# Kernel optimization log

Hardware: AMD Instinct MI355X
Metric: run time of the kernel (lower is better)

Reference implementation:

```python
import jax, jax.numpy as jnp
import numpy as np

BETA = 0.25
B, D, H, W = 32, 256, 32, 32
K = 1024


def setup_inputs() -> dict:
    key = jax.random.key(0)
    k1, k2 = jax.random.split(key)
    inputs = jax.random.normal(k1, (B, D, H, W), dtype=jnp.float32)
    # torch init: uniform(-1/K, 1/K)
    codebook = jax.random.uniform(k2, (K, D), dtype=jnp.float32,
                                  minval=-1.0 / K, maxval=1.0 / K)
    return {"inputs": inputs, "codebook": codebook}


def reference(inputs, codebook):
    b, d, h, w = inputs.shape
    # (B, C, H, W) -> (B*H*W, D)
    x = inputs.transpose(0, 2, 3, 1).reshape(b * h * w, d)
    # Squared Euclidean distances; argmin is identical to cdist argmin.
    x2 = jnp.sum(x * x, axis=1, keepdims=True)            # (N, 1)
    c2 = jnp.sum(codebook * codebook, axis=1)             # (K,)
    d2 = x2 - 2.0 * (x @ codebook.T) + c2[None, :]        # (N, K)
    idx = jnp.argmin(d2, axis=1)                          # (N,)
    q = codebook[idx].reshape(b, h, w, d).transpose(0, 3, 1, 2)  # (B, D, H, W)

    q_loss = jnp.mean((q - jax.lax.stop_gradient(inputs)) ** 2)
    e_loss = jnp.mean((jax.lax.stop_gradient(q) - inputs) ** 2)
    vq_loss = q_loss + BETA * e_loss

    # straight-through estimator
    quantized = inputs + jax.lax.stop_gradient(q - inputs)
    return quantized, q_loss, e_loss, vq_loss, idx.reshape(b, h, w)
```

## Files before the change

kernel.cpp:

```cpp
#include <hip/hip_runtime.h>
#include <cstdint>

typedef float floatx4 __attribute__((ext_vector_type(4)));
typedef _Float16 half8 __attribute__((ext_vector_type(8)));
typedef _Float16 half4v __attribute__((ext_vector_type(4)));

#define D_DIM 256
#define HW 1024
#define K_CODES 1024
#define NPIX 32768
#define NELEM 8388608

#define OFF_QLOSS 8388608
#define OFF_ELOSS 8388609
#define OFF_VQ    8388610
#define OFF_IDX   8388611

#define WS_C2      0
#define WS_CNT     4096
#define WS_LFIX    4160
#define WS_PART    4224
#define WS_FLAGPX  8320
#define WS_FLAGTOP 41088
#define WS_CBS     303232
#define FLAG_CAP   8192

#define MARGIN 2.5e-4f

__device__ __forceinline__ float np_pairwise_sq_256(const float* __restrict__ a, int stride) {
    float half[2];
#pragma unroll
    for (int h = 0; h < 2; ++h) {
        const float* p = a + (size_t)(h * 128) * stride;
        float r[8];
#pragma unroll
        for (int j = 0; j < 8; ++j) { float t = p[(size_t)j * stride]; r[j] = __fmul_rn(t, t); }
        for (int i = 8; i < 128; i += 8)
#pragma unroll
            for (int j = 0; j < 8; ++j) {
                float t = p[(size_t)(i + j) * stride];
                r[j] = __fadd_rn(r[j], __fmul_rn(t, t));
            }
        half[h] = __fadd_rn(__fadd_rn(__fadd_rn(r[0], r[1]), __fadd_rn(r[2], r[3])),
                            __fadd_rn(__fadd_rn(r[4], r[5]), __fadd_rn(r[6], r[7])));
    }
    return __fadd_rn(half[0], half[1]);
}

__global__ __launch_bounds__(256) void prep_kernel(const float* __restrict__ cb,
                                                   _Float16* __restrict__ cbs,
                                                   float* __restrict__ c2,
                                                   int* __restrict__ cnt,
                                                   double* __restrict__ lossFix) {
    int b = blockIdx.x;
    if (b < 256) {
        int idx = b * 256 + threadIdx.x;
        int c = idx >> 6;
        int d = (idx & 63) * 4;
        int s = d >> 5, q = (d >> 3) & 3, j0 = d & 7;
        int half = c >> 9, ch = (c >> 4) & 31, l15 = c & 15;
        int lane = q * 16 + l15;
        size_t o = ((((size_t)(half * 32 + ch) * 8 + s) * 64 + lane) * 8 + j0);
        floatx4 v = *(const floatx4*)(cb + (size_t)c * D_DIM + d);
        half4v h;
#pragma unroll
        for (int j = 0; j < 4; ++j) h[j] = (_Float16)(v[j] * 1024.0f);
        *(half4v*)(cbs + o) = h;
    } else {
        if (b == 256 && threadIdx.x == 0) *cnt = 0;
        if (b == 257 && threadIdx.x == 0) *lossFix = 0.0;
        int k = (b - 256) * 256 + threadIdx.x;
        c2[k] = np_pairwise_sq_256(cb + (size_t)k * D_DIM, 1);
    }
}

__device__ __forceinline__ void ins4v(float v, int k, float* S, int* I) {
    if (v < S[3]) {
        S[3] = v; I[3] = k;
#pragma unroll
        for (int j = 3; j > 0; --j) {
            if (S[j] < S[j - 1]) {
                float ts = S[j]; S[j] = S[j - 1]; S[j - 1] = ts;
                int   ti = I[j]; I[j] = I[j - 1]; I[j - 1] = ti;
            }
        }
    }
}

__global__ __launch_bounds__(256, 2) void gemm_swz(
        const float* __restrict__ x, const float* __restrict__ cb,
        const _Float16* __restrict__ cbs, const float* __restrict__ c2,
        float* __restrict__ out_idx, float* __restrict__ out_q,
        double* __restrict__ partials, int* __restrict__ cnt,
        int* __restrict__ flagPx, floatx4* __restrict__ flagTop) {
    __shared__ float scr[4][32 * 65];
    __shared__ int sidx[64];
    __shared__ double sredd[4];

    const int t = threadIdx.x;
    const int w = t >> 6;
    const int l = t & 63;
    const int l15 = l & 15;
    const int q = l >> 4;
    const int pxg = w >> 1;
    const int half = w & 1;
    const int px0 = blockIdx.x * 64;
    const int bimg = px0 >> 10;
    const int hwb = (px0 & 1023) + pxg * 32;
    const float* xb = x + (size_t)bimg * (D_DIM * HW);

    half8 A[2][8];
#pragma unroll
    for (int r = 0; r < 2; ++r) {
        float tmp[64];
#pragma unroll
        for (int s = 0; s < 8; ++s)
#pragma unroll
            for (int j = 0; j < 8; ++j)
                tmp[s * 8 + j] = xb[(size_t)(s * 32 + q * 8 + j) * HW + hwb + r * 16 + l15];
#pragma unroll
        for (int s = 0; s < 8; ++s) {
            half8 h;
#pragma unroll
            for (int j = 0; j < 8; ++j) h[j] = (_Float16)tmp[s * 8 + j];
            A[r][s] = h;
        }
    }

    const _Float16* base = cbs + (size_t)half * 131072;
    half8 B[4][8];
#pragma unroll
    for (int s = 0; s < 8; ++s) {
        B[0][s] = *(const half8*)(base + (size_t)s * 512 + l * 8);
        B[1][s] = *(const half8*)(base + 4096 + (size_t)s * 512 + l * 8);
    }
    float c2b[4];
    c2b[0] = c2[half * 512 + l15];
    c2b[1] = c2[half * 512 + 16 + l15];

    float m1[2][4], m2[2][4]; int i1[2][4], i2[2][4];
#pragma unroll
    for (int r = 0; r < 2; ++r)
#pragma unroll
        for (int a = 0; a < 4; ++a) {
            m1[r][a] = INFINITY; m2[r][a] = INFINITY; i1[r][a] = 0; i2[r][a] = 0;
        }

#pragma unroll 4
    for (int ch = 0; ch < 32; ++ch) {
        const int cur = ch & 3;
        if (ch < 30) {
            const int pf = (ch + 2) & 3;
            const _Float16* nb = base + (size_t)(ch + 2) * 4096;
#pragma unroll
            for (int s = 0; s < 8; ++s)
                B[pf][s] = *(const half8*)(nb + (size_t)s * 512 + l * 8);
            c2b[pf] = c2[half * 512 + (ch + 2) * 16 + l15];
        }
        floatx4 ac[2][2];
#pragma unroll
        for (int r = 0; r < 2; ++r)
#pragma unroll
            for (int h = 0; h < 2; ++h) ac[r][h] = floatx4{0.f, 0.f, 0.f, 0.f};
#pragma unroll
        for (int s = 0; s < 4; ++s) {
            ac[0][0] = __builtin_amdgcn_mfma_f32_16x16x32_f16(A[0][s],     B[cur][s],     ac[0][0], 0, 0, 0);
            ac[1][0] = __builtin_amdgcn_mfma_f32_16x16x32_f16(A[1][s],     B[cur][s],     ac[1][0], 0, 0, 0);
            ac[0][1] = __builtin_amdgcn_mfma_f32_16x16x32_f16(A[0][s + 4], B[cur][s + 4], ac[0][1], 0, 0, 0);
            ac[1][1] = __builtin_amdgcn_mfma_f32_16x16x32_f16(A[1][s + 4], B[cur][s + 4], ac[1][1], 0, 0, 0);
        }
        const int code = half * 512 + ch * 16 + l15;
        const float c2cur = c2b[cur];
#pragma unroll
        for (int r = 0; r < 2; ++r)
#pragma unroll
            for (int a = 0; a < 4; ++a) {
                float dot = ac[r][0][a] + ac[r][1][a];
                float s = fmaf(-0.001953125f, dot, c2cur);
                if (s < m1[r][a]) { m2[r][a] = m1[r][a]; i2[r][a] = i1[r][a]; m1[r][a] = s; i1[r][a] = code; }
                else if (s < m2[r][a]) { m2[r][a] = s; i2[r][a] = code; }
            }
    }

    const int part = half * 16 + l15;
#pragma unroll
    for (int r = 0; r < 2; ++r)
#pragma unroll
        for (int a = 0; a < 4; ++a) {
            int px = pxg * 32 + r * 16 + q * 4 + a;
            int o = part * 65 + px;
            scr[0][o] = m1[r][a];
            scr[1][o] = __int_as_float(i1[r][a]);
            scr[2][o] = m2[r][a];
            scr[3][o] = __int_as_float(i2[r][a]);
        }
    __syncthreads();
    if (t < 64) {
        float S[4] = {INFINITY, INFINITY, INFINITY, INFINITY};
        int   I[4] = {0x7fffffff, 0x7fffffff, 0x7fffffff, 0x7fffffff};
        for (int p = 0; p < 32; ++p) {
            int o = p * 65 + t;
            ins4v(scr[0][o], __float_as_int(scr[1][o]), S, I);
            ins4v(scr[2][o], __float_as_int(scr[3][o]), S, I);
        }
        int P = px0 + t;
        sidx[t] = I[0];
        out_idx[P] = (float)I[0];
        if (S[1] - S[0] <= MARGIN) {
            int pos = atomicAdd(cnt, 1);
            if (pos < FLAG_CAP) {
                flagPx[pos] = P;
                flagTop[2 * pos]     = floatx4{S[0], (float)I[0], S[1], (float)I[1]};
                flagTop[2 * pos + 1] = floatx4{S[2], (float)I[2], S[3], (float)I[3]};
            }
        }
    }
    __syncthreads();

    {
        const int dq = t >> 6;
        const int pxl = t & 63;
        const int myidx = sidx[pxl];
        const int hwofs = (px0 & 1023) + pxl;
        const float* xcol = x + (size_t)bimg * (D_DIM * HW) + hwofs;
        float* qcol = out_q + (size_t)bimg * (D_DIM * HW) + hwofs;
        const floatx4* crow = (const floatx4*)(cb + (size_t)myidx * D_DIM) + dq * 16;
        float lsum = 0.f;
#pragma unroll
        for (int i = 0; i < 16; ++i) {
            floatx4 cv = crow[i];
            int dbase = dq * 64 + i * 4;
#pragma unroll
            for (int j = 0; j < 4; ++j) {
                size_t off = (size_t)(dbase + j) * HW;
                float xv = xcol[off];
                qcol[off] = cv[j];
                float df = cv[j] - xv;
                lsum = fmaf(df, df, lsum);
            }
        }
        double ds = (double)lsum;
#pragma unroll
        for (int off = 32; off > 0; off >>= 1) ds += __shfl_down(ds, off);
        if (l == 0) sredd[w] = ds;
    }
    __syncthreads();
    if (t == 0) partials[blockIdx.x] = sredd[0] + sredd[1] + sredd[2] + sredd[3];
}

__global__ __launch_bounds__(256) void rescore_fix(
        const float* __restrict__ x, const float* __restrict__ cb,
        const float* __restrict__ c2, const int* __restrict__ cnt,
        const int* __restrict__ flagPx, const floatx4* __restrict__ flagTop,
        float* __restrict__ out_idx, float* __restrict__ out_q,
        double* __restrict__ lossFix) {
    const int wglobal = blockIdx.x * 4 + (threadIdx.x >> 6);
    const int l = threadIdx.x & 63;
    int n = *cnt; if (n > FLAG_CAP) n = FLAG_CAP;
    for (int i = wglobal; i < n; i += 1024) {
        int P = flagPx[i];
        floatx4 ta = flagTop[2 * i], tb = flagTop[2 * i + 1];
        float s1 = ta[0];
        float cs[4] = {ta[0], ta[2], tb[0], tb[2]};
        int   ck[4] = {(int)ta[1], (int)ta[3], (int)tb[1], (int)tb[3]};
        int nc = 1;
        while (nc < 4 && cs[nc] - s1 <= MARGIN) ++nc;

        const size_t colbase = (size_t)(P >> 10) * (D_DIM * HW) + (P & 1023);
        const float* xcol = x + colbase;

        float rj = 0.f;
        if (l < 16) {
            int h = l >> 3, j = l & 7;
            const float* p = xcol + (size_t)(h * 128) * HW;
            float v0 = p[(size_t)j * HW];
            rj = __fmul_rn(v0, v0);
            for (int ii = 1; ii < 16; ++ii) {
                float v = p[(size_t)(ii * 8 + j) * HW];
                rj = __fadd_rn(rj, __fmul_rn(v, v));
            }
        }
        float r0 = __shfl(rj, 0), r1 = __shfl(rj, 1), r2 = __shfl(rj, 2), r3 = __shfl(rj, 3);
        float r4 = __shfl(rj, 4), r5 = __shfl(rj, 5), r6 = __shfl(rj, 6), r7 = __shfl(rj, 7);
        float h0 = __fadd_rn(__fadd_rn(__fadd_rn(r0, r1), __fadd_rn(r2, r3)),
                             __fadd_rn(__fadd_rn(r4, r5), __fadd_rn(r6, r7)));
        r0 = __shfl(rj, 8); r1 = __shfl(rj, 9); r2 = __shfl(rj, 10); r3 = __shfl(rj, 11);
        r4 = __shfl(rj, 12); r5 = __shfl(rj, 13); r6 = __shfl(rj, 14); r7 = __shfl(rj, 15);
        float h1 = __fadd_rn(__fadd_rn(__fadd_rn(r0, r1), __fadd_rn(r2, r3)),
                             __fadd_rn(__fadd_rn(r4, r5), __fadd_rn(r6, r7)));
        float x2 = __fadd_rn(h0, h1);

        float xv[4];
#pragma unroll
        for (int u = 0; u < 4; ++u) xv[u] = xcol[(size_t)(l + u * 64) * HW];
        double accd[4] = {0.0, 0.0, 0.0, 0.0};
        for (int jc = 0; jc < nc; ++jc) {
            const float* cr = cb + (size_t)ck[jc] * D_DIM;
            double a = 0.0;
#pragma unroll
            for (int u = 0; u < 4; ++u) a += (double)xv[u] * (double)cr[l + u * 64];
#pragma unroll
            for (int off = 32; off > 0; off >>= 1) a += __shfl_xor(a, off);
            accd[jc] = a;
        }
        float bd = INFINITY; int bi = 0x7fffffff;
        for (int jc = 0; jc < nc; ++jc) {
            float mm = (float)accd[jc];
            float t1 = __fsub_rn(x2, __fmul_rn(2.0f, mm));
            float Dq = __fadd_rn(t1, c2[ck[jc]]);
            if (Dq < bd || (Dq == bd && ck[jc] < bi)) { bd = Dq; bi = ck[jc]; }
        }
        int oldI = (int)ta[1];
        if (l == 0) out_idx[P] = (float)bi;
        if (bi != oldI) {
            const float* cn = cb + (size_t)bi * D_DIM;
            const float* co = cb + (size_t)oldI * D_DIM;
            float* qcol = out_q + colbase;
            double dd = 0.0;
#pragma unroll
            for (int u = 0; u < 4; ++u) {
                int d = l + u * 64;
                float cnd = cn[d], cod = co[d];
                double dn = (double)cnd - (double)xv[u];
                double do_ = (double)cod - (double)xv[u];
                dd += dn * dn - do_ * do_;
                qcol[(size_t)d * HW] = cnd;
            }
#pragma unroll
            for (int off = 32; off > 0; off >>= 1) dd += __shfl_xor(dd, off);
            if (l == 0) atomicAdd(lossFix, dd);
        }
    }
}

__global__ __launch_bounds__(64) void finalize_loss(const double* __restrict__ partials,
                                                    const double* __restrict__ lossFix,
                                                    float* __restrict__ out) {
    double s = 0.0;
    for (int i = threadIdx.x; i < 512; i += 64) s += partials[i];
#pragma unroll
    for (int off = 32; off > 0; off >>= 1) s += __shfl_down(s, off);
    if (threadIdx.x == 0) {
        double m = (s + *lossFix) / (double)NELEM;
        out[OFF_QLOSS] = (float)m;
        out[OFF_ELOSS] = (float)m;
        out[OFF_VQ]    = (float)(1.25 * m);
    }
}

extern "C" void kernel_launch(void* const* d_in, const int* in_sizes, int n_in,
                              void* d_out, int out_size, void* d_ws, size_t ws_size,
                              hipStream_t stream) {
    const float* x  = (const float*)d_in[0];
    const float* cb = (const float*)d_in[1];
    float* out = (float*)d_out;
    char* ws = (char*)d_ws;

    float*    c2      = (float*)(ws + WS_C2);
    int*      cnt     = (int*)(ws + WS_CNT);
    double*   lossFix = (double*)(ws + WS_LFIX);
    double*   partials= (double*)(ws + WS_PART);
    int*      flagPx  = (int*)(ws + WS_FLAGPX);
    floatx4*  flagTop = (floatx4*)(ws + WS_FLAGTOP);
    _Float16* cbs     = (_Float16*)(ws + WS_CBS);

    prep_kernel<<<260, 256, 0, stream>>>(cb, cbs, c2, cnt, lossFix);
    gemm_swz<<<NPIX / 64, 256, 0, stream>>>(x, cb, cbs, c2, out + OFF_IDX, out,
                                            partials, cnt, flagPx, flagTop);
    rescore_fix<<<256, 256, 0, stream>>>(x, cb, c2, cnt, flagPx, flagTop,
                                         out + OFF_IDX, out, lossFix);
    finalize_loss<<<1, 64, 0, stream>>>(partials, lossFix, out);
}
```

Before: 170.3 us.

## Split quantize/loss epilogue into own kernel and fold finalize into rescore

Moves the codebook gather, quantized-output write and loss partial sum out of the GEMM kernel into a separate quantize_loss_kernel with 1024 smaller blocks. The finalize_loss launch is removed; the last rescore_fix block, found through an atomic done counter, reduces the partials. The aim is to shorten the register- and LDS-heavy GEMM kernel's tail and drop one launch. In exchange, the indices are re-read from global memory and one extra kernel is added.

New measurement: 193.9 us. 1.14x slower.

```diff
diff --git a/kernel.cpp b/kernel.cpp
--- a/kernel.cpp
+++ b/kernel.cpp
@@ -18,11 +18,12 @@
 
 #define WS_C2      0
 #define WS_CNT     4096
-#define WS_LFIX    4160
-#define WS_PART    4224
-#define WS_FLAGPX  8320
-#define WS_FLAGTOP 41088
-#define WS_CBS     303232
+#define WS_DONE    4160
+#define WS_LFIX    4224
+#define WS_PART    4288
+#define WS_FLAGPX  12480
+#define WS_FLAGTOP 45248
+#define WS_CBS     307392
 #define FLAG_CAP   8192
 
 #define MARGIN 2.5e-4f
@@ -51,7 +52,8 @@
                                                    _Float16* __restrict__ cbs,
                                                    float* __restrict__ c2,
                                                    int* __restrict__ cnt,
-                                                   double* __restrict__ lossFix) {
+                                                   double* __restrict__ lossFix,
+                                                   int* __restrict__ done) {
     int b = blockIdx.x;
     if (b < 256) {
         int idx = b * 256 + threadIdx.x;
@@ -69,6 +71,7 @@
     } else {
         if (b == 256 && threadIdx.x == 0) *cnt = 0;
         if (b == 257 && threadIdx.x == 0) *lossFix = 0.0;
+        if (b == 258 && threadIdx.x == 0) *done = 0;
         int k = (b - 256) * 256 + threadIdx.x;
         c2[k] = np_pairwise_sq_256(cb + (size_t)k * D_DIM, 1);
     }
@@ -88,14 +91,11 @@
 }
 
 __global__ __launch_bounds__(256, 2) void gemm_swz(
-        const float* __restrict__ x, const float* __restrict__ cb,
-        const _Float16* __restrict__ cbs, const float* __restrict__ c2,
-        float* __restrict__ out_idx, float* __restrict__ out_q,
-        double* __restrict__ partials, int* __restrict__ cnt,
-        int* __restrict__ flagPx, floatx4* __restrict__ flagTop) {
+        const float* __restrict__ x, const _Float16* __restrict__ cbs,
+        const float* __restrict__ c2, float* __restrict__ out_idx,
+        int* __restrict__ cnt, int* __restrict__ flagPx,
+        floatx4* __restrict__ flagTop) {
     __shared__ float scr[4][32 * 65];
-    __shared__ int sidx[64];
-    __shared__ double sredd[4];
 
     const int t = threadIdx.x;
     const int w = t >> 6;
@@ -204,7 +204,6 @@
             ins4v(scr[2][o], __float_as_int(scr[3][o]), S, I);
         }
         int P = px0 + t;
-        sidx[t] = I[0];
         out_idx[P] = (float)I[0];
         if (S[1] - S[0] <= MARGIN) {
             int pos = atomicAdd(cnt, 1);
@@ -215,37 +214,42 @@
             }
         }
     }
+}
+
+__global__ __launch_bounds__(256) void quantize_loss_kernel(
+        const float* __restrict__ x, const float* __restrict__ cb,
+        const float* __restrict__ out_idx, float* __restrict__ out_q,
+        double* __restrict__ partials) {
+    const int t = threadIdx.x;
+    const int pxl = t & 31;
+    const int dg = t >> 5;
+    const int P = blockIdx.x * 32 + pxl;
+    const int bimg = P >> 10, hw = P & 1023;
+    const float* xb = x + (size_t)bimg * D_DIM * HW + hw;
+    float* qb = out_q + (size_t)bimg * D_DIM * HW + hw;
+    const int myidx = (int)out_idx[P];
+    const floatx4* crow = (const floatx4*)(cb + (size_t)myidx * D_DIM) + dg * 8;
+    float lsum = 0.f;
+#pragma unroll
+    for (int i = 0; i < 8; ++i) {
+        floatx4 cv = crow[i];
+        int dbase = dg * 32 + i * 4;
+#pragma unroll
+        for (int j = 0; j < 4; ++j) {
+            size_t off = (size_t)(dbase + j) * HW;
+            float xv = xb[off];
+            qb[off] = cv[j];
+            float df = cv[j] - xv;
+            lsum = fmaf(df, df, lsum);
+        }
+    }
+    double ds = (double)lsum;
+#pragma unroll
+    for (int off = 32; off > 0; off >>= 1) ds += __shfl_down(ds, off);
+    __shared__ double sred[4];
+    if ((t & 63) == 0) sred[t >> 6] = ds;
     __syncthreads();
-
-    {
-        const int dq = t >> 6;
-        const int pxl = t & 63;
-        const int myidx = sidx[pxl];
-        const int hwofs = (px0 & 1023) + pxl;
-        const float* xcol = x + (size_t)bimg * (D_DIM * HW) + hwofs;
-        float* qcol = out_q + (size_t)bimg * (D_DIM * HW) + hwofs;
-        const floatx4* crow = (const floatx4*)(cb + (size_t)myidx * D_DIM) + dq * 16;
-        float lsum = 0.f;
-#pragma unroll
-        for (int i = 0; i < 16; ++i) {
-            floatx4 cv = crow[i];
-            int dbase = dq * 64 + i * 4;
-#pragma unroll
-            for (int j = 0; j < 4; ++j) {
-                size_t off = (size_t)(dbase + j) * HW;
-                float xv = xcol[off];
-                qcol[off] = cv[j];
-                float df = cv[j] - xv;
-                lsum = fmaf(df, df, lsum);
-            }
-        }
-        double ds = (double)lsum;
-#pragma unroll
-        for (int off = 32; off > 0; off >>= 1) ds += __shfl_down(ds, off);
-        if (l == 0) sredd[w] = ds;
-    }
-    __syncthreads();
-    if (t == 0) partials[blockIdx.x] = sredd[0] + sredd[1] + sredd[2] + sredd[3];
+    if (t == 0) partials[blockIdx.x] = sred[0] + sred[1] + sred[2] + sred[3];
 }
 
 __global__ __launch_bounds__(256) void rescore_fix(
@@ -253,7 +257,8 @@
         const float* __restrict__ c2, const int* __restrict__ cnt,
         const int* __restrict__ flagPx, const floatx4* __restrict__ flagTop,
         float* __restrict__ out_idx, float* __restrict__ out_q,
-        double* __restrict__ lossFix) {
+        double* __restrict__ lossFix, double* __restrict__ partials,
+        int* __restrict__ done, float* __restrict__ out) {
     const int wglobal = blockIdx.x * 4 + (threadIdx.x >> 6);
     const int l = threadIdx.x & 63;
     int n = *cnt; if (n > FLAG_CAP) n = FLAG_CAP;
@@ -331,20 +336,27 @@
             if (l == 0) atomicAdd(lossFix, dd);
         }
     }
-}
-
-__global__ __launch_bounds__(64) void finalize_loss(const double* __restrict__ partials,
-                                                    const double* __restrict__ lossFix,
-                                                    float* __restrict__ out) {
-    double s = 0.0;
-    for (int i = threadIdx.x; i < 512; i += 64) s += partials[i];
-#pragma unroll
-    for (int off = 32; off > 0; off >>= 1) s += __shfl_down(s, off);
-    if (threadIdx.x == 0) {
-        double m = (s + *lossFix) / (double)NELEM;
-        out[OFF_QLOSS] = (float)m;
-        out[OFF_ELOSS] = (float)m;
-        out[OFF_VQ]    = (float)(1.25 * m);
+
+    __shared__ bool amLast;
+    __threadfence();
+    if (threadIdx.x == 0)
+        amLast = (atomicAdd(done, 1) == (int)gridDim.x - 1);
+    __syncthreads();
+    if (amLast) {
+        double s = 0.0;
+        for (int i = threadIdx.x; i < 1024; i += 256) s += partials[i];
+        __shared__ double sred[4];
+#pragma unroll
+        for (int off = 32; off > 0; off >>= 1) s += __shfl_down(s, off);
+        if ((threadIdx.x & 63) == 0) sred[threadIdx.x >> 6] = s;
+        __syncthreads();
+        if (threadIdx.x == 0) {
+            double fix = atomicAdd(lossFix, 0.0);
+            double m = (sred[0] + sred[1] + sred[2] + sred[3] + fix) / (double)NELEM;
+            out[OFF_QLOSS] = (float)m;
+            out[OFF_ELOSS] = (float)m;
+            out[OFF_VQ]    = (float)(1.25 * m);
+        }
     }
 }
 
@@ -358,16 +370,19 @@
 
     float*    c2      = (float*)(ws + WS_C2);
     int*      cnt     = (int*)(ws + WS_CNT);
+    int*      done    = (int*)(ws + WS_DONE);
     double*   lossFix = (double*)(ws + WS_LFIX);
     double*   partials= (double*)(ws + WS_PART);
     int*      flagPx  = (int*)(ws + WS_FLAGPX);
     floatx4*  flagTop = (floatx4*)(ws + WS_FLAGTOP);
     _Float16* cbs     = (_Float16*)(ws + WS_CBS);
 
-    prep_kernel<<<260, 256, 0, stream>>>(cb, cbs, c2, cnt, lossFix);
-    gemm_swz<<<NPIX / 64, 256, 0, stream>>>(x, cb, cbs, c2, out + OFF_IDX, out,
-                                            partials, cnt, flagPx, flagTop);
+    prep_kernel<<<260, 256, 0, stream>>>(cb, cbs, c2, cnt, lossFix, done);
+    gemm_swz<<<NPIX / 64, 256, 0, stream>>>(x, cbs, c2, out + OFF_IDX,
+                                            cnt, flagPx, flagTop);
+    quantize_loss_kernel<<<NPIX / 32, 256, 0, stream>>>(x, cb, out + OFF_IDX,
+                                                        out, partials);
     rescore_fix<<<256, 256, 0, stream>>>(x, cb, c2, cnt, flagPx, flagTop,
-                                         out + OFF_IDX, out, lossFix);
-    finalize_loss<<<1, 64, 0, stream>>>(partials, lossFix, out);
-}
+                                         out + OFF_IDX, out, lossFix, partials,
+                                         done, out);
+}
```
